# Performance work log

Hardware: AMD Instinct MI355X
Metric: run time of the kernel (lower is better)

The kernel has to match this reference:

```python
import jax, jax.numpy as jnp
import numpy as np

DIM_K = 512  # scale factor denominator sqrt(dim_k)


def setup_inputs() -> dict:
    key = jax.random.key(0)
    ks = jax.random.split(key, 7)
    B, S, D = 2, 4096, 512
    scale = 1.0 / np.sqrt(D)
    return {
        "x1": jax.random.normal(ks[0], (B, S, D), dtype=jnp.float32),
        "Wq": jax.random.normal(ks[1], (D, D), dtype=jnp.float32) * scale,
        "bq": jax.random.normal(ks[2], (D,), dtype=jnp.float32) * scale,
        "Wk": jax.random.normal(ks[3], (D, D), dtype=jnp.float32) * scale,
        "bk": jax.random.normal(ks[4], (D,), dtype=jnp.float32) * scale,
        "Wv": jax.random.normal(ks[5], (D, D), dtype=jnp.float32) * scale,
        "bv": jax.random.normal(ks[6], (D,), dtype=jnp.float32) * scale,
    }


def reference(x1, Wq, bq, Wk, bk, Wv, bv):
    # torch Linear: y = x @ W.T + b, then ReLU on each of Q/K/V
    q = jax.nn.relu(jnp.einsum("bsd,ed->bse", x1, Wq) + bq)  # [B,S,D]
    k = jax.nn.relu(jnp.einsum("bsd,ed->bse", x1, Wk) + bk)
    v = jax.nn.relu(jnp.einsum("bsd,ed->bse", x1, Wv) + bv)
    scores = jnp.einsum("bsd,btd->bst", q, k) / jnp.sqrt(jnp.float32(DIM_K))
    attn = jax.nn.softmax(scores, axis=-1)
    # dropout_p = 0.0 -> identity (deterministic)
    return jnp.einsum("bst,btd->bsd", attn, v)
```

## Files before the change

### kernel.cpp

```cpp
#include <hip/hip_runtime.h>

typedef float f32x4 __attribute__((ext_vector_type(4)));
typedef short s16x8 __attribute__((ext_vector_type(8)));
typedef unsigned short u16x4 __attribute__((ext_vector_type(4)));
typedef unsigned short ushort_t;

__device__ __forceinline__ unsigned short f2bf(float f) {
    union { float f; unsigned int u; } v; v.f = f;
    unsigned int r = (v.u + 0x7fffu + ((v.u >> 16) & 1u)) >> 16;
    return (unsigned short)r;
}
__device__ __forceinline__ unsigned short tbf(float f) {
    union { float f; unsigned int u; } v; v.f = f;
    return (unsigned short)(v.u >> 16);
}
__device__ __forceinline__ float bf2f(unsigned short b) {
    union { unsigned int u; float f; } v; v.u = ((unsigned int)b) << 16;
    return v.f;
}

__device__ __forceinline__ f32x4 mfma_bf16(s16x8 a, s16x8 b, f32x4 c) {
    return __builtin_amdgcn_mfma_f32_16x16x32_bf16(a, b, c, 0, 0, 0);
}

__device__ __forceinline__ void gl_lds16(const void* g, void* l) {
    __builtin_amdgcn_global_load_lds(
        (const __attribute__((address_space(1))) unsigned int*)g,
        (__attribute__((address_space(3))) unsigned int*)l, 16, 0, 0);
}

#define QSCALE 0.06375871469f
#define FIXED_M 18.0f

__global__ __launch_bounds__(256) void qkv_proj_fused(
    const float* __restrict__ x,
    const float* __restrict__ Wq, const float* __restrict__ bq,
    const float* __restrict__ Wk, const float* __restrict__ bk,
    const float* __restrict__ Wv, const float* __restrict__ bv,
    ushort_t* __restrict__ qkv_ws)
{
    const int mblk = blockIdx.x;
    const int nblk = blockIdx.y;

    __shared__ ushort_t a_lds[128][40];
    __shared__ ushort_t b_lds[3][128][40];

    const int tid  = threadIdx.x;
    const int lane = tid & 63;
    const int wave = tid >> 6;
    const int wr = wave >> 1, wc = wave & 1;

    f32x4 acc[3][4][4] = {};

    for (int k0 = 0; k0 < 512; k0 += 32) {
        #pragma unroll
        for (int i = 0; i < 4; i++) {
            const int chunk = i * 256 + tid;
            const int row = chunk >> 3, c4 = (chunk & 7) * 4;
            const float4 v = *reinterpret_cast<const float4*>(
                x + (size_t)(mblk * 128 + row) * 512 + k0 + c4);
            u16x4 pk;
            pk[0] = f2bf(v.x); pk[1] = f2bf(v.y);
            pk[2] = f2bf(v.z); pk[3] = f2bf(v.w);
            *reinterpret_cast<u16x4*>(&a_lds[row][c4]) = pk;
        }
        #pragma unroll
        for (int wsel = 0; wsel < 3; wsel++) {
            const float* W = (wsel == 0) ? Wq : (wsel == 1) ? Wk : Wv;
            #pragma unroll
            for (int i = 0; i < 4; i++) {
                const int chunk = i * 256 + tid;
                const int row = chunk >> 3, c4 = (chunk & 7) * 4;
                const float4 v = *reinterpret_cast<const float4*>(
                    W + (size_t)(nblk * 128 + row) * 512 + k0 + c4);
                u16x4 pk;
                pk[0] = f2bf(v.x); pk[1] = f2bf(v.y);
                pk[2] = f2bf(v.z); pk[3] = f2bf(v.w);
                *reinterpret_cast<u16x4*>(&b_lds[wsel][row][c4]) = pk;
            }
        }
        __syncthreads();

        s16x8 af[4];
        #pragma unroll
        for (int m = 0; m < 4; m++)
            af[m] = *reinterpret_cast<const s16x8*>(
                &a_lds[wr * 64 + m * 16 + (lane & 15)][(lane >> 4) * 8]);
        #pragma unroll
        for (int wsel = 0; wsel < 3; wsel++) {
            s16x8 bf[4];
            #pragma unroll
            for (int n = 0; n < 4; n++)
                bf[n] = *reinterpret_cast<const s16x8*>(
                    &b_lds[wsel][wc * 64 + n * 16 + (lane & 15)][(lane >> 4) * 8]);
            #pragma unroll
            for (int m = 0; m < 4; m++)
                #pragma unroll
                for (int n = 0; n < 4; n++)
                    acc[wsel][m][n] = mfma_bf16(af[m], bf[n], acc[wsel][m][n]);
        }
        __syncthreads();
    }

    #pragma unroll
    for (int wsel = 0; wsel < 3; wsel++) {
        const float* bias = (wsel == 0) ? bq : (wsel == 1) ? bk : bv;
        ushort_t* out = qkv_ws + (size_t)wsel * (8192u * 512u);
        const float scale = (wsel == 0) ? QSCALE : 1.0f;
        if (wsel == 2) {
            #pragma unroll
            for (int n = 0; n < 4; n++) {
                const int col = nblk * 128 + wc * 64 + n * 16 + (lane & 15);
                const float b = bias[col];
                #pragma unroll
                for (int m = 0; m < 4; m++) {
                    const int rowb = mblk * 128 + wr * 64 + m * 16 + (lane >> 4) * 4;
                    const int batch = rowb >> 12, sr = rowb & 4095;
                    u16x4 pk;
                    #pragma unroll
                    for (int j = 0; j < 4; j++)
                        pk[j] = f2bf(fmaxf(acc[2][m][n][j] + b, 0.0f));
                    *reinterpret_cast<u16x4*>(out + (size_t)batch * 512 * 4096 +
                                              (size_t)col * 4096 + sr) = pk;
                }
            }
        } else {
            #pragma unroll
            for (int n = 0; n < 4; n++) {
                const int col = nblk * 128 + wc * 64 + n * 16 + (lane & 15);
                const float b = bias[col];
                #pragma unroll
                for (int m = 0; m < 4; m++) {
                    #pragma unroll
                    for (int j = 0; j < 4; j++) {
                        const int row = mblk * 128 + wr * 64 + m * 16 + (lane >> 4) * 4 + j;
                        float v = fmaxf(acc[wsel][m][n][j] + b, 0.0f) * scale;
                        out[(size_t)row * 512 + col] = f2bf(v);
                    }
                }
            }
        }
    }
}

__global__ __launch_bounds__(512, 2) void attn_v10(
    const ushort_t* __restrict__ qkv_ws,
    ushort_t* __restrict__ opart, float* __restrict__ ml,
    float* __restrict__ out, int SP, int NK)
{
    const int combo = blockIdx.x;
    const int batch = combo / SP;
    const int split = combo % SP;
    const int qblk  = blockIdx.y;
    const int tid = threadIdx.x, lane = tid & 63, wave = tid >> 6;
    const int kv00 = split * (4096 / SP);

    const ushort_t* q_ws  = qkv_ws;
    const ushort_t* k_ws  = qkv_ws + (size_t)8192 * 512;
    const ushort_t* vt_ws = qkv_ws + (size_t)2 * 8192 * 512;
    const size_t base  = (size_t)batch * 4096 * 512;
    const size_t vbase = (size_t)batch * 512 * 4096;

    __shared__ ushort_t k_lds[2][32 * 512];
    __shared__ ushort_t vt_lds[2][512 * 32];
    __shared__ ushort_t p_lds[128][36];
    __shared__ float l_lds[128];

    const int g = lane >> 4;
    const int l15 = lane & 15;

    s16x8 qf[16];
    {
        const int qrow0 = qblk * 128 + wave * 16 + l15;
        const ushort_t* qp = q_ws + base + (size_t)qrow0 * 512 + g * 8;
        #pragma unroll
        for (int ks = 0; ks < 16; ks++)
            qf[ks] = *reinterpret_cast<const s16x8*>(qp + ks * 32);
    }

    const f32x4 zf = {0.f, 0.f, 0.f, 0.f};
    f32x4 o[8][4];
    #pragma unroll
    for (int rf = 0; rf < 8; rf++)
        #pragma unroll
        for (int cf = 0; cf < 4; cf++) o[rf][cf] = zf;
    float lrow[4] = {0.f, 0.f, 0.f, 0.f};

#define STAGE(BUF, KV0)                                                         \
    do {                                                                        \
        _Pragma("unroll")                                                       \
        for (int i = 0; i < 4; i++) {                                           \
            const int C   = i * 8192 + tid * 16;                                \
            const int row = C >> 10;                                            \
            const int Lc  = (C & 1023) ^ ((row & 7) << 4);                      \
            gl_lds16(k_ws + base + (size_t)((KV0) + row) * 512 + (Lc >> 1),     \
                     (char*)&k_lds[BUF][0] + C);                                \
        }                                                                       \
        _Pragma("unroll")                                                       \
        for (int i = 0; i < 4; i++) {                                           \
            const int C    = i * 8192 + tid * 16;                               \
            const int drow = C >> 6;                                            \
            const int gc   = (C >> 4) & 3;                                      \
            const int gl   = gc ^ ((drow >> 1) & 3);                            \
            gl_lds16(vt_ws + vbase + (size_t)drow * 4096 + (KV0) + gl * 8,      \
                     (char*)&vt_lds[BUF][0] + C);                               \
        }                                                                       \
    } while (0)

    STAGE(0, kv00);
    asm volatile("s_waitcnt vmcnt(0)" ::: "memory");
    __builtin_amdgcn_s_barrier();

    int cur = 0;
    for (int t = 0; t < NK; ++t) {
        if (t + 1 < NK) STAGE(cur ^ 1, kv00 + (t + 1) * 32);

        const char* kb = (const char*)&k_lds[cur][0];
        f32x4 s0 = zf, s1 = zf;
        #pragma unroll
        for (int ks = 0; ks < 16; ++ks) {
            const int xr = (ks * 64 + g * 16) ^ ((l15 & 7) << 4);
            const s16x8 kf0 = *reinterpret_cast<const s16x8*>(kb + l15 * 1024 + xr);
            const s16x8 kf1 = *reinterpret_cast<const s16x8*>(kb + (16 + l15) * 1024 + xr);
            s0 = mfma_bf16(qf[ks], kf0, s0);
            s1 = mfma_bf16(qf[ks], kf1, s1);
        }

        #pragma unroll
        for (int j = 0; j < 4; j++) {
            const float p0 = exp2f(s0[j] - FIXED_M);
            const float p1 = exp2f(s1[j] - FIXED_M);
            lrow[j] += p0 + p1;
            const int pr = wave * 16 + g * 4 + j;
            p_lds[pr][l15]      = tbf(p0);
            p_lds[pr][16 + l15] = tbf(p1);
        }

        asm volatile("s_waitcnt lgkmcnt(0)" ::: "memory");
        __builtin_amdgcn_sched_barrier(0);
        __builtin_amdgcn_s_barrier();
        __builtin_amdgcn_sched_barrier(0);

        {
            const char* vb = (const char*)&vt_lds[cur][0];
            s16x8 vf[4];
            #pragma unroll
            for (int cf = 0; cf < 4; cf++) {
                const int d = wave * 64 + cf * 16 + l15;
                vf[cf] = *reinterpret_cast<const s16x8*>(
                    vb + d * 64 + ((g * 16) ^ (((d >> 1) & 3) << 4)));
            }
            #pragma unroll
            for (int rf = 0; rf < 8; rf++) {
                const s16x8 pf = *reinterpret_cast<const s16x8*>(
                    &p_lds[rf * 16 + l15][g * 8]);
                #pragma unroll
                for (int cf = 0; cf < 4; cf++)
                    o[rf][cf] = mfma_bf16(pf, vf[cf], o[rf][cf]);
            }
        }

        asm volatile("s_waitcnt vmcnt(0) lgkmcnt(0)" ::: "memory");
        __builtin_amdgcn_sched_barrier(0);
        __builtin_amdgcn_s_barrier();
        __builtin_amdgcn_sched_barrier(0);
        cur ^= 1;
    }
#undef STAGE

    #pragma unroll
    for (int j = 0; j < 4; j++) {
        #pragma unroll
        for (int msk = 8; msk >= 1; msk >>= 1)
            lrow[j] += __shfl_xor(lrow[j], msk, 64);
    }
    if (l15 == 0) {
        #pragma unroll
        for (int j = 0; j < 4; j++)
            l_lds[wave * 16 + g * 4 + j] = lrow[j];
    }
    __builtin_amdgcn_s_barrier();

    const int qrowb = qblk * 128;
    if (opart != nullptr) {
        const size_t prow8k = (size_t)batch * 4096;
        if (l15 == 0) {
            #pragma unroll
            for (int j = 0; j < 4; j++) {
                const size_t r = prow8k + qrowb + wave * 16 + g * 4 + j;
                ml[((size_t)split * 8192 + r) * 2 + 1] = lrow[j];
            }
        }
        ushort_t* op = opart + (size_t)split * 8192 * 512;
        #pragma unroll
        for (int rf = 0; rf < 8; rf++) {
            #pragma unroll
            for (int cf = 0; cf < 4; cf++) {
                #pragma unroll
                for (int j = 0; j < 4; j++) {
                    const size_t r = prow8k + qrowb + rf * 16 + g * 4 + j;
                    op[r * 512 + wave * 64 + cf * 16 + l15] = f2bf(o[rf][cf][j]);
                }
            }
        }
    } else {
        #pragma unroll
        for (int rf = 0; rf < 8; rf++) {
            #pragma unroll
            for (int j = 0; j < 4; j++) {
                const int rl = rf * 16 + g * 4 + j;
                const float inv = 1.0f / l_lds[rl];
                #pragma unroll
                for (int cf = 0; cf < 4; cf++) {
                    out[base + (size_t)(qrowb + rl) * 512 + wave * 64 + cf * 16 + l15]
                        = o[rf][cf][j] * inv;
                }
            }
        }
    }
}

__global__ __launch_bounds__(256) void merge_kernel(
    const ushort_t* __restrict__ opart, const float* __restrict__ ml,
    float* __restrict__ out, int SP)
{
    const int row  = blockIdx.x * 4 + (threadIdx.x >> 6);
    const int lane = threadIdx.x & 63;

    float denom = 0.0f;
    for (int s = 0; s < SP; s++)
        denom += ml[((size_t)s * 8192 + row) * 2 + 1];
    const float inv = 1.0f / denom;

    float acc[8] = {};
    for (int s = 0; s < SP; s++) {
        const s16x8 v = *reinterpret_cast<const s16x8*>(
            opart + ((size_t)s * 8192 + row) * 512 + lane * 8);
        #pragma unroll
        for (int i = 0; i < 8; i++)
            acc[i] += bf2f((ushort_t)v[i]);
    }
    float* dst = out + (size_t)row * 512 + lane * 8;
    #pragma unroll
    for (int i = 0; i < 8; i++) dst[i] = acc[i] * inv;
}

extern "C" void kernel_launch(void* const* d_in, const int* in_sizes, int n_in,
                              void* d_out, int out_size, void* d_ws, size_t ws_size,
                              hipStream_t stream) {
    const float* x  = (const float*)d_in[0];
    const float* Wq = (const float*)d_in[1];
    const float* bq = (const float*)d_in[2];
    const float* Wk = (const float*)d_in[3];
    const float* bk = (const float*)d_in[4];
    const float* Wv = (const float*)d_in[5];
    const float* bv = (const float*)d_in[6];
    float* out = (float*)d_out;
    ushort_t* qkv = (ushort_t*)d_ws;
    (void)in_sizes; (void)n_in; (void)out_size;

    const size_t qkv_bytes = 3ull * 8192 * 512 * 2;

    int SP = 0;
    if (ws_size >= qkv_bytes + 4ull * (8388608 + 65536)) SP = 4;
    else if (ws_size >= qkv_bytes + 2ull * (8388608 + 65536)) SP = 2;
    else if (ws_size >= qkv_bytes + 1ull * (8388608 + 65536)) SP = 1;

    dim3 gp(64, 4);
    qkv_proj_fused<<<gp, 256, 0, stream>>>(x, Wq, bq, Wk, bk, Wv, bv, qkv);

    if (SP > 0) {
        ushort_t* opart = qkv + 3ull * 8192 * 512;
        float* ml = (float*)(opart + (size_t)SP * 8192 * 512);
        dim3 ga(2 * SP, 32);
        attn_v10<<<ga, 512, 0, stream>>>(qkv, opart, ml, out, SP, (4096 / SP) / 32);
        merge_kernel<<<2048, 256, 0, stream>>>(opart, ml, out, SP);
    } else {
        dim3 ga(2, 32);
        attn_v10<<<ga, 512, 0, stream>>>(qkv, nullptr, nullptr, out, 1, 128);
    }
}
```

Measured before the change: 150.6 us.

## Pre-cast inputs to bf16, add split projection GEMM, reorder attention prefetch

Adds a cast kernel that converts x and the three weight matrices to bf16 in the workspace. A new projection GEMM then uses async global-to-LDS double-buffered loads, one grid z-slice per Q/K/V, and writes V transposed with packed stores. The attention kernel now issues its next-tile prefetch after the QK/softmax barrier and uses partial vmcnt waits, aiming to overlap loads with the PV MFMAs. These changes cost an extra kernel launch and an extra round trip of x through memory, and they reuse the opart workspace for the bf16 copies.

New measurement: 179.7 us. +19.4%, slower.

```diff
diff --git a/kernel.cpp b/kernel.cpp
--- a/kernel.cpp
+++ b/kernel.cpp
@@ -3,6 +3,7 @@
 typedef float f32x4 __attribute__((ext_vector_type(4)));
 typedef short s16x8 __attribute__((ext_vector_type(8)));
 typedef unsigned short u16x4 __attribute__((ext_vector_type(4)));
+typedef unsigned short u16x8 __attribute__((ext_vector_type(8)));
 typedef unsigned short ushort_t;
 
 __device__ __forceinline__ unsigned short f2bf(float f) {
@@ -31,6 +32,141 @@
 
 #define QSCALE 0.06375871469f
 #define FIXED_M 18.0f
+
+__global__ __launch_bounds__(256) void cast_kernel(
+    const float* __restrict__ x,
+    const float* __restrict__ Wq, const float* __restrict__ Wk,
+    const float* __restrict__ Wv,
+    ushort_t* __restrict__ xb, ushort_t* __restrict__ wb)
+{
+    const int i = blockIdx.x * 256 + threadIdx.x;
+    const float* src;
+    ushort_t* dst;
+    size_t off;
+    if (i < 524288) {
+        src = x; dst = xb; off = (size_t)i;
+    } else {
+        const int j = i - 524288;
+        const int w = j >> 15;
+        off = (size_t)(j & 32767);
+        src = (w == 0) ? Wq : (w == 1) ? Wk : Wv;
+        dst = wb + (size_t)w * 262144;
+    }
+    const float4 v0 = *reinterpret_cast<const float4*>(src + off * 8);
+    const float4 v1 = *reinterpret_cast<const float4*>(src + off * 8 + 4);
+    u16x8 p;
+    p[0] = f2bf(v0.x); p[1] = f2bf(v0.y); p[2] = f2bf(v0.z); p[3] = f2bf(v0.w);
+    p[4] = f2bf(v1.x); p[5] = f2bf(v1.y); p[6] = f2bf(v1.z); p[7] = f2bf(v1.w);
+    *reinterpret_cast<u16x8*>(dst + off * 8) = p;
+}
+
+__global__ __launch_bounds__(256) void proj_bf16(
+    const ushort_t* __restrict__ xb, const ushort_t* __restrict__ wb,
+    const float* __restrict__ bq, const float* __restrict__ bk,
+    const float* __restrict__ bv,
+    ushort_t* __restrict__ qkv_ws)
+{
+    const int mblk  = blockIdx.x;
+    const int nblk  = blockIdx.y;
+    const int which = blockIdx.z;
+
+    const ushort_t* W = wb + (size_t)which * 262144;
+    const float* bias = (which == 0) ? bq : (which == 1) ? bk : bv;
+    ushort_t* out = qkv_ws + (size_t)which * (8192u * 512u);
+    const float scale = (which == 0) ? QSCALE : 1.0f;
+
+    __shared__ ushort_t a_lds[2][128 * 32];
+    __shared__ ushort_t b_lds[2][128 * 32];
+
+    const int tid  = threadIdx.x;
+    const int lane = tid & 63;
+    const int wave = tid >> 6;
+    const int wr = wave >> 1, wc = wave & 1;
+    const int g = lane >> 4, l15 = lane & 15;
+
+    f32x4 acc[4][4] = {};
+
+#define PSTAGE(BUF, K0)                                                         \
+    do {                                                                        \
+        _Pragma("unroll")                                                       \
+        for (int i = 0; i < 2; i++) {                                           \
+            const int c = i * 256 + tid;                                        \
+            gl_lds16(xb + (size_t)(mblk * 128 + (c >> 2)) * 512 + (K0) + (c & 3) * 8, \
+                     (char*)&a_lds[BUF][0] + c * 16);                           \
+        }                                                                       \
+        _Pragma("unroll")                                                       \
+        for (int i = 0; i < 2; i++) {                                           \
+            const int c = i * 256 + tid;                                        \
+            gl_lds16(W + (size_t)(nblk * 128 + (c >> 2)) * 512 + (K0) + (c & 3) * 8, \
+                     (char*)&b_lds[BUF][0] + c * 16);                           \
+        }                                                                       \
+    } while (0)
+
+    PSTAGE(0, 0);
+    asm volatile("s_waitcnt vmcnt(0)" ::: "memory");
+    __builtin_amdgcn_s_barrier();
+
+    int cur = 0;
+    for (int t = 0; t < 16; ++t) {
+        if (t + 1 < 16) PSTAGE(cur ^ 1, (t + 1) * 32);
+
+        s16x8 af[4], bf[4];
+        #pragma unroll
+        for (int m = 0; m < 4; m++)
+            af[m] = *reinterpret_cast<const s16x8*>(
+                (const char*)&a_lds[cur][0] + (wr * 64 + m * 16 + l15) * 64 + g * 16);
+        #pragma unroll
+        for (int n = 0; n < 4; n++)
+            bf[n] = *reinterpret_cast<const s16x8*>(
+                (const char*)&b_lds[cur][0] + (wc * 64 + n * 16 + l15) * 64 + g * 16);
+
+        #pragma unroll
+        for (int m = 0; m < 4; m++)
+            #pragma unroll
+            for (int n = 0; n < 4; n++)
+                acc[m][n] = mfma_bf16(af[m], bf[n], acc[m][n]);
+
+        asm volatile("s_waitcnt vmcnt(0) lgkmcnt(0)" ::: "memory");
+        __builtin_amdgcn_sched_barrier(0);
+        __builtin_amdgcn_s_barrier();
+        cur ^= 1;
+    }
+#undef PSTAGE
+
+    if (which == 2) {
+        #pragma unroll
+        for (int n = 0; n < 4; n++) {
+            const int col = nblk * 128 + wc * 64 + n * 16 + l15;
+            const float b = bias[col];
+            #pragma unroll
+            for (int m = 0; m < 4; m++) {
+                const int rowb = mblk * 128 + wr * 64 + m * 16 + g * 4;
+                const int batch = rowb >> 12, sr = rowb & 4095;
+                u16x4 pk;
+                #pragma unroll
+                for (int j = 0; j < 4; j++)
+                    pk[j] = f2bf(fmaxf(acc[m][n][j] + b, 0.0f));
+                *reinterpret_cast<u16x4*>(out + (size_t)batch * 512 * 4096 +
+                                          (size_t)col * 4096 + sr) = pk;
+            }
+        }
+    } else {
+        #pragma unroll
+        for (int n = 0; n < 4; n++) {
+            const int col = nblk * 128 + wc * 64 + n * 16 + l15;
+            const float b = bias[col];
+            #pragma unroll
+            for (int m = 0; m < 4; m++) {
+                #pragma unroll
+                for (int j = 0; j < 4; j++) {
+                    const int row = mblk * 128 + wr * 64 + m * 16 + g * 4 + j;
+                    float v = fmaxf(acc[m][n][j] + b, 0.0f) * scale;
+                    out[(size_t)row * 512 + col] = f2bf(v);
+                }
+            }
+        }
+    }
+}
 
 __global__ __launch_bounds__(256) void qkv_proj_fused(
     const float* __restrict__ x,
@@ -143,7 +279,7 @@
     }
 }
 
-__global__ __launch_bounds__(512, 2) void attn_v10(
+__global__ __launch_bounds__(512, 2) void attn_v13(
     const ushort_t* __restrict__ qkv_ws,
     ushort_t* __restrict__ opart, float* __restrict__ ml,
     float* __restrict__ out, int SP, int NK)
@@ -208,13 +344,12 @@
     } while (0)
 
     STAGE(0, kv00);
-    asm volatile("s_waitcnt vmcnt(0)" ::: "memory");
+    asm volatile("s_waitcnt vmcnt(4)" ::: "memory");
+    __builtin_amdgcn_sched_barrier(0);
     __builtin_amdgcn_s_barrier();
 
     int cur = 0;
     for (int t = 0; t < NK; ++t) {
-        if (t + 1 < NK) STAGE(cur ^ 1, kv00 + (t + 1) * 32);
-
         const char* kb = (const char*)&k_lds[cur][0];
         f32x4 s0 = zf, s1 = zf;
         #pragma unroll
@@ -236,10 +371,12 @@
             p_lds[pr][16 + l15] = tbf(p1);
         }
 
-        asm volatile("s_waitcnt lgkmcnt(0)" ::: "memory");
+        asm volatile("s_waitcnt vmcnt(0) lgkmcnt(0)" ::: "memory");
         __builtin_amdgcn_sched_barrier(0);
         __builtin_amdgcn_s_barrier();
         __builtin_amdgcn_sched_barrier(0);
+
+        if (t + 1 < NK) STAGE(cur ^ 1, kv00 + (t + 1) * 32);
 
         {
             const char* vb = (const char*)&vt_lds[cur][0];
@@ -260,7 +397,10 @@
             }
         }
 
-        asm volatile("s_waitcnt vmcnt(0) lgkmcnt(0)" ::: "memory");
+        if (t + 1 < NK)
+            asm volatile("s_waitcnt vmcnt(4) lgkmcnt(0)" ::: "memory");
+        else
+            asm volatile("s_waitcnt vmcnt(0) lgkmcnt(0)" ::: "memory");
         __builtin_amdgcn_sched_barrier(0);
         __builtin_amdgcn_s_barrier();
         __builtin_amdgcn_sched_barrier(0);
@@ -366,17 +506,26 @@
     else if (ws_size >= qkv_bytes + 2ull * (8388608 + 65536)) SP = 2;
     else if (ws_size >= qkv_bytes + 1ull * (8388608 + 65536)) SP = 1;
 
-    dim3 gp(64, 4);
-    qkv_proj_fused<<<gp, 256, 0, stream>>>(x, Wq, bq, Wk, bk, Wv, bv, qkv);
+    ushort_t* opart = qkv + 3ull * 8192 * 512;
+
+    if (SP >= 2) {
+        ushort_t* xb = opart;
+        ushort_t* wb = opart + (size_t)8192 * 512;
+        cast_kernel<<<2432, 256, 0, stream>>>(x, Wq, Wk, Wv, xb, wb);
+        dim3 gp(64, 4, 3);
+        proj_bf16<<<gp, 256, 0, stream>>>(xb, wb, bq, bk, bv, qkv);
+    } else {
+        dim3 gp(64, 4);
+        qkv_proj_fused<<<gp, 256, 0, stream>>>(x, Wq, bq, Wk, bk, Wv, bv, qkv);
+    }
 
     if (SP > 0) {
-        ushort_t* opart = qkv + 3ull * 8192 * 512;
         float* ml = (float*)(opart + (size_t)SP * 8192 * 512);
         dim3 ga(2 * SP, 32);
-        attn_v10<<<ga, 512, 0, stream>>>(qkv, opart, ml, out, SP, (4096 / SP) / 32);
+        attn_v13<<<ga, 512, 0, stream>>>(qkv, opart, ml, out, SP, (4096 / SP) / 32);
         merge_kernel<<<2048, 256, 0, stream>>>(opart, ml, out, SP);
     } else {
         dim3 ga(2, 32);
-        attn_v10<<<ga, 512, 0, stream>>>(qkv, nullptr, nullptr, out, 1, 128);
-    }
-}
+        attn_v13<<<ga, 512, 0, stream>>>(qkv, nullptr, nullptr, out, 1, 128);
+    }
+}
```
